# Performance work log

Measured on AMD Instinct MI355X. Metric: run time of the kernel, lower is better.

The kernel has to match this reference:

```python
import jax, jax.numpy as jnp
import numpy as np

DIM = 2048
N_HEADS = 16
HEAD_DIM = 128
EPS = 1e-6


def setup_inputs() -> dict:
    key = jax.random.key(0)
    ks = jax.random.split(key, 8)
    b, gf, gh, gw = 1, 8, 16, 24
    s = gf * gh * gw
    c = HEAD_DIM // 2
    w = lambda k: 0.02 * jax.random.normal(k, (DIM, DIM), jnp.float32)
    return {
        "x": jax.random.normal(ks[0], (b, s, DIM), jnp.float32),
        "freqs_angle": jax.random.normal(ks[1], (1024, c), jnp.float32),
        "Wq": w(ks[2]), "bq": jnp.zeros((DIM,), jnp.float32),
        "Wk": w(ks[3]), "bk": jnp.zeros((DIM,), jnp.float32),
        "Wv": w(ks[4]), "bv": jnp.zeros((DIM,), jnp.float32),
        "Wo": w(ks[5]), "bo": jnp.zeros((DIM,), jnp.float32),
        "gq": jnp.ones((DIM,), jnp.float32),
        "gk": jnp.ones((DIM,), jnp.float32),
        "seq_len": s, "grid_f": gf, "grid_h": gh, "grid_w": gw,
    }


def _rms(t, g):
    return t * jax.lax.rsqrt(jnp.mean(t * t, axis=-1, keepdims=True) + EPS) * g


def _grid_angles(freqs_angle, gf, gh, gw, c):
    # band split [c - 2*(c//3), c//3, c//3] as in rope_apply
    cf = c - 2 * (c // 3)
    ch = cw = c // 3
    af = freqs_angle[:gf, :cf]            # [F, cf]
    ah = freqs_angle[:gh, cf:cf + ch]     # [H, ch]
    aw = freqs_angle[:gw, cf + ch:c]      # [W, cw]
    ang = jnp.concatenate([
        jnp.broadcast_to(af[:, None, None, :], (gf, gh, gw, cf)),
        jnp.broadcast_to(ah[None, :, None, :], (gf, gh, gw, ch)),
        jnp.broadcast_to(aw[None, None, :, :], (gf, gh, gw, cw)),
    ], axis=-1)
    return ang.reshape(gf * gh * gw, c)   # [s, c]


def reference(x, freqs_angle, Wq, bq, Wk, bk, Wv, bv, Wo, bo, gq, gk,
              seq_len, grid_f, grid_h, grid_w):
    b, s, _ = x.shape
    n, d = N_HEADS, HEAD_DIM
    c = d // 2
    ang = _grid_angles(freqs_angle, grid_f, grid_h, grid_w, c)
    cos = jnp.cos(ang)[None, :, None, :]  # [1, s, 1, c]
    sin = jnp.sin(ang)[None, :, None, :]

    def rope(t):  # complex multiply on (even, odd) = (real, imag) pairs
        te, to = t[..., 0::2], t[..., 1::2]
        return jnp.stack([te * cos - to * sin, te * sin + to * cos], axis=-1).reshape(t.shape)

    q = _rms(x @ Wq.T + bq, gq).reshape(b, s, n, d)
    k = _rms(x @ Wk.T + bk, gk).reshape(b, s, n, d)
    v = (x @ Wv.T + bv).reshape(b, s, n, d)
    q, k = rope(q), rope(k)

    scale = np.float32(1.0 / np.sqrt(d))
    scores = jnp.einsum('bqnd,bknd->bnqk', q, k) * scale
    p = jax.nn.softmax(scores, axis=-1)
    o = jnp.einsum('bnqk,bknd->bqnd', p, v).reshape(b, s, n * d)
    return o @ Wo.T + bo
```

## Files before the change

### kernel.cpp

```cpp
#include <hip/hip_runtime.h>
#include <stdint.h>
#include <stddef.h>

typedef __bf16 bf16_t;
typedef __bf16 bf16x8 __attribute__((ext_vector_type(8)));
typedef __bf16 bf16x4 __attribute__((ext_vector_type(4)));
typedef __bf16 bf16x2 __attribute__((ext_vector_type(2)));
typedef float  f32x4  __attribute__((ext_vector_type(4)));

#define SEQ   3072
#define DIMD  2048
#define NH    16
#define HD    128
#define QKVN  6144

__device__ __forceinline__ void async16(const bf16_t* g, bf16_t* l) {
  __builtin_amdgcn_global_load_lds((const __attribute__((address_space(1))) uint32_t*)g,
                                   (__attribute__((address_space(3))) uint32_t*)l, 16, 0, 0);
}

__global__ __launch_bounds__(256) void cvt_all(const float* __restrict__ x,
                                               const float* __restrict__ Wq,
                                               const float* __restrict__ Wk,
                                               const float* __restrict__ Wv,
                                               const float* __restrict__ Wo,
                                               const float* __restrict__ bq,
                                               const float* __restrict__ bk,
                                               const float* __restrict__ bv,
                                               bf16_t* __restrict__ xb,
                                               bf16_t* __restrict__ Wqkvb,
                                               bf16_t* __restrict__ Wob,
                                               float* __restrict__ bqkv) {
  const int b = blockIdx.x;
  const float* src; bf16_t* dst; int off;
  if (b < 3072)       { src = x;  dst = xb;              off = b; }
  else if (b < 5120)  { src = Wq; dst = Wqkvb;           off = b - 3072; }
  else if (b < 7168)  { src = Wk; dst = Wqkvb + 4194304; off = b - 5120; }
  else if (b < 9216)  { src = Wv; dst = Wqkvb + 8388608; off = b - 7168; }
  else if (b < 11264) { src = Wo; dst = Wob;             off = b - 9216; }
  else {
    int t = (b - 11264) * 256 + threadIdx.x;
    float v;
    if (t < 2048)      v = bq[t];
    else if (t < 4096) v = bk[t - 2048];
    else               v = bv[t - 4096];
    bqkv[t] = v;
    return;
  }
  const int idx = (off * 256 + threadIdx.x) * 8;
  const float4 a = *(const float4*)(src + idx);
  const float4 c = *(const float4*)(src + idx + 4);
  bf16x8 o;
  o[0] = (bf16_t)a.x; o[1] = (bf16_t)a.y; o[2] = (bf16_t)a.z; o[3] = (bf16_t)a.w;
  o[4] = (bf16_t)c.x; o[5] = (bf16_t)c.y; o[6] = (bf16_t)c.z; o[7] = (bf16_t)c.w;
  *(bf16x8*)(dst + idx) = o;
}

template<bool OUT_BF16>
__global__ __launch_bounds__(256, 2) void gemm_nt(const bf16_t* __restrict__ A,
                                                  const bf16_t* __restrict__ B,
                                                  const float* __restrict__ bias,
                                                  void* __restrict__ Cout,
                                                  int M, int N, int K) {
  __shared__ __align__(16) bf16_t As[128 * 64];
  __shared__ __align__(16) bf16_t Bs[128 * 64];
  const int t = threadIdx.x;
  const int lane = t & 63, wave = t >> 6;
  const int quad = lane >> 4, l15 = lane & 15;
  const int wy = wave >> 1, wx = wave & 1;
  const size_t bm = (size_t)blockIdx.y * 128, bn = (size_t)blockIdx.x * 128;
  const bf16_t* Ab = A + bm * K;
  const bf16_t* Bb = B + bn * K;
  f32x4 acc[4][4] = {};
  int srow[4], scol[4];
#pragma unroll
  for (int r = 0; r < 4; r++) {
    int L = r * 256 + t;
    int row = L >> 3, cp = L & 7;
    srow[r] = row;
    scol[r] = (cp ^ (row & 7)) * 8;
  }
  for (int k0 = 0; k0 < K; k0 += 64) {
    __syncthreads();
#pragma unroll
    for (int r = 0; r < 4; r++)
      async16(Ab + (size_t)srow[r] * K + k0 + scol[r], &As[(r * 256 + t) * 8]);
#pragma unroll
    for (int r = 0; r < 4; r++)
      async16(Bb + (size_t)srow[r] * K + k0 + scol[r], &Bs[(r * 256 + t) * 8]);
    __syncthreads();
#pragma unroll
    for (int ks = 0; ks < 2; ks++) {
      bf16x8 af[4], bfv[4];
#pragma unroll
      for (int i = 0; i < 4; i++) {
        int row = wy * 64 + i * 16 + l15;
        af[i] = *(const bf16x8*)&As[row * 64 + (((ks * 4 + quad) ^ (row & 7)) * 8)];
      }
#pragma unroll
      for (int j = 0; j < 4; j++) {
        int row = wx * 64 + j * 16 + l15;
        bfv[j] = *(const bf16x8*)&Bs[row * 64 + (((ks * 4 + quad) ^ (row & 7)) * 8)];
      }
#pragma unroll
      for (int i = 0; i < 4; i++)
#pragma unroll
        for (int j = 0; j < 4; j++)
          acc[i][j] = __builtin_amdgcn_mfma_f32_16x16x32_bf16(af[i], bfv[j], acc[i][j], 0, 0, 0);
    }
  }
#pragma unroll
  for (int i = 0; i < 4; i++) {
#pragma unroll
    for (int j = 0; j < 4; j++) {
      size_t row = bm + wy * 64 + i * 16 + quad * 4;
      size_t col = bn + wx * 64 + j * 16 + l15;
      float bb = bias[col];
#pragma unroll
      for (int r = 0; r < 4; r++) {
        float v = acc[i][j][r] + bb;
        if (OUT_BF16) ((bf16_t*)Cout)[(row + r) * N + col] = (bf16_t)v;
        else          ((float*)Cout)[(row + r) * N + col] = v;
      }
    }
  }
}

__global__ __launch_bounds__(256) void rmsrope(bf16_t* __restrict__ qkv,
                                               bf16_t* __restrict__ pk,
                                               const float* __restrict__ gq,
                                               const float* __restrict__ gk,
                                               const float* __restrict__ freqs) {
  const int s = blockIdx.x, t = threadIdx.x;
  bf16_t* row = qkv + (size_t)s * QKVN;
  bf16x8 qv = *(const bf16x8*)&row[t * 8];
  bf16x8 kv = *(const bf16x8*)&row[2048 + t * 8];
  float qf[8], kf[8];
  float qs = 0.f, ks2 = 0.f;
#pragma unroll
  for (int i = 0; i < 8; i++) {
    qf[i] = (float)qv[i]; qs  += qf[i] * qf[i];
    kf[i] = (float)kv[i]; ks2 += kf[i] * kf[i];
  }
#pragma unroll
  for (int m = 1; m < 64; m <<= 1) {
    qs  += __shfl_xor(qs, m);
    ks2 += __shfl_xor(ks2, m);
  }
  __shared__ float red[2][4];
  const int wave = t >> 6, lane = t & 63;
  if (lane == 0) { red[0][wave] = qs; red[1][wave] = ks2; }
  __syncthreads();
  qs  = red[0][0] + red[0][1] + red[0][2] + red[0][3];
  ks2 = red[1][0] + red[1][1] + red[1][2] + red[1][3];
  const float qsc = rsqrtf(qs  / 2048.f + 1e-6f) * 0.12751745f;
  const float ksc = rsqrtf(ks2 / 2048.f + 1e-6f);
  const int sf = s / 384, rem = s - sf * 384;
  const int sh = rem / 24, sw = rem - sh * 24;
  bf16x8 qo, ko;
#pragma unroll
  for (int u = 0; u < 4; u++) {
    const int col = t * 8 + 2 * u;
    const int i = (col >> 1) & 63;
    const int frow = (i < 22) ? sf : ((i < 43) ? sh : sw);
    const float ang = freqs[frow * 64 + i];
    float sn, cs;
    __sincosf(ang, &sn, &cs);
    float te = qf[2 * u]     * qsc * gq[col];
    float to = qf[2 * u + 1] * qsc * gq[col + 1];
    qo[2 * u]     = (bf16_t)(te * cs - to * sn);
    qo[2 * u + 1] = (bf16_t)(te * sn + to * cs);
    te = kf[2 * u]     * ksc * gk[col];
    to = kf[2 * u + 1] * ksc * gk[col + 1];
    ko[2 * u]     = (bf16_t)(te * cs - to * sn);
    ko[2 * u + 1] = (bf16_t)(te * sn + to * cs);
  }
  *(bf16x8*)&row[t * 8] = qo;
  *(bf16x8*)&pk[((size_t)(t >> 4) * SEQ + s) * HD + (t & 15) * 8] = ko;
}

__global__ __launch_bounds__(256) void vtrans(const bf16_t* __restrict__ qkv,
                                              bf16_t* __restrict__ pvt) {
  __shared__ bf16_t tile[128][65];
  const int h = blockIdx.y;
  const int s0 = blockIdx.x * 64;
  const int t = threadIdx.x;
#pragma unroll
  for (int r = 0; r < 4; r++) {
    int L = r * 256 + t, s = L >> 4, cp = L & 15;
    bf16x8 v = *(const bf16x8*)&qkv[(size_t)(s0 + s) * QKVN + 4096 + h * HD + cp * 8];
#pragma unroll
    for (int i = 0; i < 8; i++) tile[cp * 8 + i][s] = v[i];
  }
  __syncthreads();
#pragma unroll
  for (int r = 0; r < 4; r++) {
    int L = r * 256 + t, d = L >> 3, c = L & 7;
    bf16x8 o;
#pragma unroll
    for (int i = 0; i < 8; i++) o[i] = tile[d][c * 8 + i];
    *(bf16x8*)&pvt[((size_t)h * HD + d) * SEQ + s0 + c * 8] = o;
  }
}

#define STAGE_KV(BUF, KV1) do {                                              \
    _Pragma("unroll")                                                        \
    for (int r = 0; r < 5; r++) {                                            \
      int L = r * 192 + t;                                                   \
      async16(pkh + (size_t)(KV1) * HD + koff[r], &Ks[BUF][L * 8]);          \
      async16(pvh + (KV1) + voff[r], &Vt[BUF][L * 8]);                       \
    }                                                                        \
    if (t < 64) {                                                            \
      int L = 5 * 192 + t;                                                   \
      async16(pkh + (size_t)(KV1) * HD + koff[5], &Ks[BUF][L * 8]);          \
      async16(pvh + (KV1) + voff[5], &Vt[BUF][L * 8]);                       \
    }                                                                        \
  } while (0)

__global__ __launch_bounds__(192, 2) void flash_attn(const bf16_t* __restrict__ qkv,
                                                     const bf16_t* __restrict__ pk,
                                                     const bf16_t* __restrict__ pvt,
                                                     bf16_t* __restrict__ ob) {
  __shared__ __align__(16) bf16_t Ks[2][64 * 128];
  __shared__ __align__(16) bf16_t Vt[2][128 * 64];
  __shared__ __align__(16) bf16_t Ps[3][32 * 64];
  const int h = blockIdx.y, qt = blockIdx.x;
  const int s0 = qt * 96;
  const int t = threadIdx.x, wave = t >> 6, lane = t & 63;
  const int quad = lane >> 4, l15 = lane & 15;
  const int wq = wave * 32;
  const bf16_t* pkh = pk  + (size_t)h * (SEQ * HD);
  const bf16_t* pvh = pvt + (size_t)h * (HD * SEQ);
  int koff[6], voff[6];
#pragma unroll
  for (int r = 0; r < 6; r++) {
    int L = r * 192 + t;
    int krow = L >> 4, kc = (L & 15) ^ (krow & 7);
    koff[r] = krow * HD + kc * 8;
    int vd = L >> 3, vc = (L & 7) ^ (vd & 7);
    voff[r] = vd * SEQ + vc * 8;
  }
  bf16x8 qfr[2][4];
#pragma unroll
  for (int tj = 0; tj < 2; tj++)
#pragma unroll
    for (int ks = 0; ks < 4; ks++)
      qfr[tj][ks] = *(const bf16x8*)&qkv[(size_t)(s0 + wq + tj * 16 + l15) * QKVN + h * HD + ks * 32 + quad * 8];
  f32x4 oacc[2][8] = {};
  float m_run[2] = {-3e38f, -3e38f}, l_run[2] = {0.f, 0.f};
  STAGE_KV(0, 0);
  for (int kt = 0; kt < SEQ / 64; kt++) {
    const int cur = kt & 1;
    __syncthreads();
    if (kt + 1 < SEQ / 64) STAGE_KV(cur ^ 1, (kt + 1) * 64);
    f32x4 st[4][2] = {};
#pragma unroll
    for (int ks = 0; ks < 4; ks++) {
      bf16x8 kfr[4];
#pragma unroll
      for (int ti = 0; ti < 4; ti++) {
        const int kr = ti * 16 + l15;
        kfr[ti] = *(const bf16x8*)&Ks[cur][kr * 128 + (((ks * 4 + quad) ^ (kr & 7)) * 8)];
      }
#pragma unroll
      for (int ti = 0; ti < 4; ti++)
#pragma unroll
        for (int tj = 0; tj < 2; tj++)
          st[ti][tj] = __builtin_amdgcn_mfma_f32_16x16x32_bf16(kfr[ti], qfr[tj][ks], st[ti][tj], 0, 0, 0);
    }
    float mt[2] = {-3e38f, -3e38f};
#pragma unroll
    for (int ti = 0; ti < 4; ti++)
#pragma unroll
      for (int tj = 0; tj < 2; tj++)
#pragma unroll
        for (int r = 0; r < 4; r++)
          mt[tj] = fmaxf(mt[tj], st[ti][tj][r]);
    float al[2]; bool resc[2];
#pragma unroll
    for (int tj = 0; tj < 2; tj++) {
      mt[tj] = fmaxf(mt[tj], __shfl_xor(mt[tj], 16));
      mt[tj] = fmaxf(mt[tj], __shfl_xor(mt[tj], 32));
      if (__all(mt[tj] <= m_run[tj] + 11.5f)) {
        al[tj] = 1.f; resc[tj] = false;
      } else {
        const float mn = fmaxf(m_run[tj], mt[tj]);
        al[tj] = __builtin_amdgcn_exp2f(m_run[tj] - mn);
        m_run[tj] = mn;
        resc[tj] = true;
      }
    }
    float lt[2] = {0.f, 0.f};
#pragma unroll
    for (int ti = 0; ti < 4; ti++)
#pragma unroll
      for (int tj = 0; tj < 2; tj++) {
        bf16x4 pv;
#pragma unroll
        for (int r = 0; r < 4; r++) {
          const float p = __builtin_amdgcn_exp2f(st[ti][tj][r] - m_run[tj]);
          pv[r] = (bf16_t)p;
          lt[tj] += (float)pv[r];
        }
        const int q = tj * 16 + l15;
        const int cp2 = (ti * 2 + (quad >> 1)) ^ (q & 7);
        *(bf16x4*)&Ps[wave][q * 64 + cp2 * 8 + (quad & 1) * 4] = pv;
      }
#pragma unroll
    for (int tj = 0; tj < 2; tj++) {
      lt[tj] += __shfl_xor(lt[tj], 16);
      lt[tj] += __shfl_xor(lt[tj], 32);
      l_run[tj] = l_run[tj] * al[tj] + lt[tj];
    }
#pragma unroll
    for (int ti = 0; ti < 2; ti++) {
      if (resc[ti]) {
        float a0 = __shfl(al[ti], quad * 4 + 0);
        float a1 = __shfl(al[ti], quad * 4 + 1);
        float a2 = __shfl(al[ti], quad * 4 + 2);
        float a3 = __shfl(al[ti], quad * 4 + 3);
#pragma unroll
        for (int dj = 0; dj < 8; dj++) {
          oacc[ti][dj][0] *= a0; oacc[ti][dj][1] *= a1;
          oacc[ti][dj][2] *= a2; oacc[ti][dj][3] *= a3;
        }
      }
    }
#pragma unroll
    for (int ks = 0; ks < 2; ks++) {
      bf16x8 pf[2], vf[8];
#pragma unroll
      for (int ti = 0; ti < 2; ti++) {
        const int q = ti * 16 + l15;
        pf[ti] = *(const bf16x8*)&Ps[wave][q * 64 + (((ks * 4 + quad) ^ (q & 7)) * 8)];
      }
#pragma unroll
      for (int dj = 0; dj < 8; dj++) {
        const int d = dj * 16 + l15;
        vf[dj] = *(const bf16x8*)&Vt[cur][d * 64 + (((ks * 4 + quad) ^ (d & 7)) * 8)];
      }
#pragma unroll
      for (int ti = 0; ti < 2; ti++)
#pragma unroll
        for (int dj = 0; dj < 8; dj++)
          oacc[ti][dj] = __builtin_amdgcn_mfma_f32_16x16x32_bf16(pf[ti], vf[dj], oacc[ti][dj], 0, 0, 0);
    }
  }
#pragma unroll
  for (int ti = 0; ti < 2; ti++) {
    float li[4];
#pragma unroll
    for (int r = 0; r < 4; r++) li[r] = 1.f / __shfl(l_run[ti], quad * 4 + r);
#pragma unroll
    for (int dj = 0; dj < 8; dj++)
#pragma unroll
      for (int r = 0; r < 4; r++) {
        const float v = oacc[ti][dj][r] * li[r];
        ob[(size_t)(s0 + wq + ti * 16 + quad * 4 + r) * DIMD + h * HD + dj * 16 + l15] = (bf16_t)v;
      }
  }
}

extern "C" void kernel_launch(void* const* d_in, const int* in_sizes, int n_in,
                              void* d_out, int out_size, void* d_ws, size_t ws_size,
                              hipStream_t stream) {
  (void)in_sizes; (void)n_in; (void)out_size;
  const float* x     = (const float*)d_in[0];
  const float* freqs = (const float*)d_in[1];
  const float* Wq    = (const float*)d_in[2];
  const float* bq    = (const float*)d_in[3];
  const float* Wk    = (const float*)d_in[4];
  const float* bk    = (const float*)d_in[5];
  const float* Wv    = (const float*)d_in[6];
  const float* bv    = (const float*)d_in[7];
  const float* Wo    = (const float*)d_in[8];
  const float* bo    = (const float*)d_in[9];
  const float* gq    = (const float*)d_in[10];
  const float* gk    = (const float*)d_in[11];

  char* w = (char*)d_ws;
  bf16_t* xb    = (bf16_t*)(w);
  bf16_t* Wqkvb = (bf16_t*)(w + 12582912);
  bf16_t* Wob   = (bf16_t*)(w + 37748736);
  bf16_t* qkvb  = (bf16_t*)(w + 46137344);
  bf16_t* obuf  = (bf16_t*)(w + 83886080);
  float*  bqkv  = (float*) (w + 96468992);
  bf16_t* pk    = (bf16_t*)(w);
  bf16_t* pvt   = (bf16_t*)(w + 12582912);
  if (ws_size < (size_t)96493568) return;

  cvt_all<<<11288, 256, 0, stream>>>(x, Wq, Wk, Wv, Wo, bq, bk, bv, xb, Wqkvb, Wob, bqkv);

  gemm_nt<true><<<dim3(48, 24), 256, 0, stream>>>(xb, Wqkvb, bqkv, qkvb, SEQ, QKVN, DIMD);
  rmsrope<<<3072, 256, 0, stream>>>(qkvb, pk, gq, gk, freqs);
  vtrans<<<dim3(48, NH), 256, 0, stream>>>(qkvb, pvt);
  flash_attn<<<dim3(32, NH), 192, 0, stream>>>(qkvb, pk, pvt, obuf);
  gemm_nt<false><<<dim3(16, 24), 256, 0, stream>>>(obuf, Wob, bo, (float*)d_out, SEQ, DIMD, DIMD);
}
```

Measured before the change: 432.8 us.

## Switch flash attention to 32x32x16 MFMA with register-resident P and MFMA row sums

Rewrites the attention inner loop to use 32x32x16 bf16 MFMAs, computing S^T so the probability tile can be rearranged into A-operand fragments in registers with cross-half lane shuffles. This drops the per-wave P shared-memory round trip and its bank traffic. The row-sum is computed by an extra MFMA against a ones vector rather than scalar adds and shuffles, and s_setprio hints are added around the MFMA phases. The cost is more accumulator registers (f32x16 tiles) and an extra MFMA per PV step, which may hurt occupancy at two blocks per CU.

```diff
diff --git a/kernel.cpp b/kernel.cpp
--- a/kernel.cpp
+++ b/kernel.cpp
@@ -7,6 +7,7 @@
 typedef __bf16 bf16x4 __attribute__((ext_vector_type(4)));
 typedef __bf16 bf16x2 __attribute__((ext_vector_type(2)));
 typedef float  f32x4  __attribute__((ext_vector_type(4)));
+typedef float  f32x16 __attribute__((ext_vector_type(16)));
 
 #define SEQ   3072
 #define DIMD  2048
@@ -223,14 +224,13 @@
                                                      bf16_t* __restrict__ ob) {
   __shared__ __align__(16) bf16_t Ks[2][64 * 128];
   __shared__ __align__(16) bf16_t Vt[2][128 * 64];
-  __shared__ __align__(16) bf16_t Ps[3][32 * 64];
-  const int h = blockIdx.y, qt = blockIdx.x;
+  const int hh = blockIdx.y, qt = blockIdx.x;
   const int s0 = qt * 96;
   const int t = threadIdx.x, wave = t >> 6, lane = t & 63;
-  const int quad = lane >> 4, l15 = lane & 15;
+  const int l31 = lane & 31, hl = lane >> 5;
   const int wq = wave * 32;
-  const bf16_t* pkh = pk  + (size_t)h * (SEQ * HD);
-  const bf16_t* pvh = pvt + (size_t)h * (HD * SEQ);
+  const bf16_t* pkh = pk  + (size_t)hh * (SEQ * HD);
+  const bf16_t* pvh = pvt + (size_t)hh * (HD * SEQ);
   int koff[6], voff[6];
 #pragma unroll
   for (int r = 0; r < 6; r++) {
@@ -240,124 +240,101 @@
     int vd = L >> 3, vc = (L & 7) ^ (vd & 7);
     voff[r] = vd * SEQ + vc * 8;
   }
-  bf16x8 qfr[2][4];
-#pragma unroll
-  for (int tj = 0; tj < 2; tj++)
-#pragma unroll
-    for (int ks = 0; ks < 4; ks++)
-      qfr[tj][ks] = *(const bf16x8*)&qkv[(size_t)(s0 + wq + tj * 16 + l15) * QKVN + h * HD + ks * 32 + quad * 8];
-  f32x4 oacc[2][8] = {};
-  float m_run[2] = {-3e38f, -3e38f}, l_run[2] = {0.f, 0.f};
+  bf16x8 qfr[8];
+#pragma unroll
+  for (int ks = 0; ks < 8; ks++)
+    qfr[ks] = *(const bf16x8*)&qkv[(size_t)(s0 + wq + l31) * QKVN + hh * HD + ks * 16 + hl * 8];
+  bf16x8 vones;
+#pragma unroll
+  for (int i = 0; i < 8; i++) vones[i] = (bf16_t)1.0f;
+  f32x16 oacc[4] = {};
+  f32x16 lacc = {};
+  float m_run = -3e38f;
   STAGE_KV(0, 0);
   for (int kt = 0; kt < SEQ / 64; kt++) {
     const int cur = kt & 1;
     __syncthreads();
     if (kt + 1 < SEQ / 64) STAGE_KV(cur ^ 1, (kt + 1) * 64);
-    f32x4 st[4][2] = {};
-#pragma unroll
-    for (int ks = 0; ks < 4; ks++) {
-      bf16x8 kfr[4];
-#pragma unroll
-      for (int ti = 0; ti < 4; ti++) {
-        const int kr = ti * 16 + l15;
-        kfr[ti] = *(const bf16x8*)&Ks[cur][kr * 128 + (((ks * 4 + quad) ^ (kr & 7)) * 8)];
+    f32x16 st0 = {}, st1 = {};
+    __builtin_amdgcn_s_setprio(1);
+#pragma unroll
+    for (int ks = 0; ks < 8; ks++) {
+      const int r1 = 32 + l31;
+      bf16x8 k0 = *(const bf16x8*)&Ks[cur][l31 * 128 + (((ks * 2 + hl) ^ (l31 & 7)) * 8)];
+      bf16x8 k1 = *(const bf16x8*)&Ks[cur][r1 * 128 + (((ks * 2 + hl) ^ (r1 & 7)) * 8)];
+      st0 = __builtin_amdgcn_mfma_f32_32x32x16_bf16(k0, qfr[ks], st0, 0, 0, 0);
+      st1 = __builtin_amdgcn_mfma_f32_32x32x16_bf16(k1, qfr[ks], st1, 0, 0, 0);
+    }
+    __builtin_amdgcn_s_setprio(0);
+    float mt = st0[0];
+#pragma unroll
+    for (int r = 1; r < 16; r++) mt = fmaxf(mt, st0[r]);
+#pragma unroll
+    for (int r = 0; r < 16; r++) mt = fmaxf(mt, st1[r]);
+    mt = fmaxf(mt, __shfl_xor(mt, 32));
+    if (!__all(mt <= m_run + 11.5f)) {
+      const float mn = fmaxf(m_run, mt);
+      const float al = __builtin_amdgcn_exp2f(m_run - mn);
+      m_run = mn;
+#pragma unroll
+      for (int r = 0; r < 16; r++) {
+        const float a = __shfl(al, (r & 3) + 8 * (r >> 2) + 4 * hl);
+        lacc[r] *= a;
+#pragma unroll
+        for (int dj = 0; dj < 4; dj++) oacc[dj][r] *= a;
       }
-#pragma unroll
-      for (int ti = 0; ti < 4; ti++)
-#pragma unroll
-        for (int tj = 0; tj < 2; tj++)
-          st[ti][tj] = __builtin_amdgcn_mfma_f32_16x16x32_bf16(kfr[ti], qfr[tj][ks], st[ti][tj], 0, 0, 0);
-    }
-    float mt[2] = {-3e38f, -3e38f};
-#pragma unroll
-    for (int ti = 0; ti < 4; ti++)
-#pragma unroll
-      for (int tj = 0; tj < 2; tj++)
-#pragma unroll
-        for (int r = 0; r < 4; r++)
-          mt[tj] = fmaxf(mt[tj], st[ti][tj][r]);
-    float al[2]; bool resc[2];
-#pragma unroll
-    for (int tj = 0; tj < 2; tj++) {
-      mt[tj] = fmaxf(mt[tj], __shfl_xor(mt[tj], 16));
-      mt[tj] = fmaxf(mt[tj], __shfl_xor(mt[tj], 32));
-      if (__all(mt[tj] <= m_run[tj] + 11.5f)) {
-        al[tj] = 1.f; resc[tj] = false;
-      } else {
-        const float mn = fmaxf(m_run[tj], mt[tj]);
-        al[tj] = __builtin_amdgcn_exp2f(m_run[tj] - mn);
-        m_run[tj] = mn;
-        resc[tj] = true;
-      }
-    }
-    float lt[2] = {0.f, 0.f};
-#pragma unroll
-    for (int ti = 0; ti < 4; ti++)
-#pragma unroll
-      for (int tj = 0; tj < 2; tj++) {
-        bf16x4 pv;
-#pragma unroll
-        for (int r = 0; r < 4; r++) {
-          const float p = __builtin_amdgcn_exp2f(st[ti][tj][r] - m_run[tj]);
-          pv[r] = (bf16_t)p;
-          lt[tj] += (float)pv[r];
-        }
-        const int q = tj * 16 + l15;
-        const int cp2 = (ti * 2 + (quad >> 1)) ^ (q & 7);
-        *(bf16x4*)&Ps[wave][q * 64 + cp2 * 8 + (quad & 1) * 4] = pv;
-      }
-#pragma unroll
-    for (int tj = 0; tj < 2; tj++) {
-      lt[tj] += __shfl_xor(lt[tj], 16);
-      lt[tj] += __shfl_xor(lt[tj], 32);
-      l_run[tj] = l_run[tj] * al[tj] + lt[tj];
-    }
-#pragma unroll
-    for (int ti = 0; ti < 2; ti++) {
-      if (resc[ti]) {
-        float a0 = __shfl(al[ti], quad * 4 + 0);
-        float a1 = __shfl(al[ti], quad * 4 + 1);
-        float a2 = __shfl(al[ti], quad * 4 + 2);
-        float a3 = __shfl(al[ti], quad * 4 + 3);
-#pragma unroll
-        for (int dj = 0; dj < 8; dj++) {
-          oacc[ti][dj][0] *= a0; oacc[ti][dj][1] *= a1;
-          oacc[ti][dj][2] *= a2; oacc[ti][dj][3] *= a3;
-        }
-      }
-    }
-#pragma unroll
-    for (int ks = 0; ks < 2; ks++) {
-      bf16x8 pf[2], vf[8];
-#pragma unroll
-      for (int ti = 0; ti < 2; ti++) {
-        const int q = ti * 16 + l15;
-        pf[ti] = *(const bf16x8*)&Ps[wave][q * 64 + (((ks * 4 + quad) ^ (q & 7)) * 8)];
-      }
-#pragma unroll
-      for (int dj = 0; dj < 8; dj++) {
-        const int d = dj * 16 + l15;
-        vf[dj] = *(const bf16x8*)&Vt[cur][d * 64 + (((ks * 4 + quad) ^ (d & 7)) * 8)];
-      }
-#pragma unroll
-      for (int ti = 0; ti < 2; ti++)
-#pragma unroll
-        for (int dj = 0; dj < 8; dj++)
-          oacc[ti][dj] = __builtin_amdgcn_mfma_f32_16x16x32_bf16(pf[ti], vf[dj], oacc[ti][dj], 0, 0, 0);
-    }
-  }
-#pragma unroll
-  for (int ti = 0; ti < 2; ti++) {
-    float li[4];
-#pragma unroll
-    for (int r = 0; r < 4; r++) li[r] = 1.f / __shfl(l_run[ti], quad * 4 + r);
-#pragma unroll
-    for (int dj = 0; dj < 8; dj++)
-#pragma unroll
-      for (int r = 0; r < 4; r++) {
-        const float v = oacc[ti][dj][r] * li[r];
-        ob[(size_t)(s0 + wq + ti * 16 + quad * 4 + r) * DIMD + h * HD + dj * 16 + l15] = (bf16_t)v;
-      }
+    }
+    uint32_t c0[8], c1[8];
+#pragma unroll
+    for (int m = 0; m < 8; m++) {
+      bf16x2 w0, w1;
+      w0[0] = (bf16_t)__builtin_amdgcn_exp2f(st0[2 * m]     - m_run);
+      w0[1] = (bf16_t)__builtin_amdgcn_exp2f(st0[2 * m + 1] - m_run);
+      w1[0] = (bf16_t)__builtin_amdgcn_exp2f(st1[2 * m]     - m_run);
+      w1[1] = (bf16_t)__builtin_amdgcn_exp2f(st1[2 * m + 1] - m_run);
+      c0[m] = __builtin_bit_cast(uint32_t, w0);
+      c1[m] = __builtin_bit_cast(uint32_t, w1);
+    }
+    union U8 { uint32_t u[4]; bf16x8 v; } afr0, afr1, afr2, afr3;
+#define BUILD_AFR(DST, CB, B) do {                                           \
+      uint32_t sA = hl ? CB[(B) + 0] : CB[(B) + 2];                          \
+      uint32_t sB = hl ? CB[(B) + 1] : CB[(B) + 3];                          \
+      uint32_t rA = (uint32_t)__shfl_xor((int)sA, 32);                       \
+      uint32_t rB = (uint32_t)__shfl_xor((int)sB, 32);                       \
+      DST.u[0] = hl ? rA : CB[(B) + 0];                                      \
+      DST.u[1] = hl ? rB : CB[(B) + 1];                                      \
+      DST.u[2] = hl ? CB[(B) + 2] : rA;                                      \
+      DST.u[3] = hl ? CB[(B) + 3] : rB;                                      \
+    } while (0)
+    BUILD_AFR(afr0, c0, 0);
+    BUILD_AFR(afr1, c0, 4);
+    BUILD_AFR(afr2, c1, 0);
+    BUILD_AFR(afr3, c1, 4);
+#undef BUILD_AFR
+    __builtin_amdgcn_s_setprio(1);
+#define PV_STEP(AFR, S) do {                                                            \
+      lacc = __builtin_amdgcn_mfma_f32_32x32x16_bf16(AFR.v, vones, lacc, 0, 0, 0);      \
+      _Pragma("unroll")                                                                 \
+      for (int dj = 0; dj < 4; dj++) {                                                  \
+        const int row = dj * 32 + l31;                                                  \
+        bf16x8 vf = *(const bf16x8*)&Vt[cur][row * 64 + ((((S) * 2 + hl) ^ (row & 7)) * 8)]; \
+        oacc[dj] = __builtin_amdgcn_mfma_f32_32x32x16_bf16(AFR.v, vf, oacc[dj], 0, 0, 0);    \
+      }                                                                                 \
+    } while (0)
+    PV_STEP(afr0, 0);
+    PV_STEP(afr1, 1);
+    PV_STEP(afr2, 2);
+    PV_STEP(afr3, 3);
+#undef PV_STEP
+    __builtin_amdgcn_s_setprio(0);
+  }
+#pragma unroll
+  for (int r = 0; r < 16; r++) {
+    const float li = 1.f / lacc[r];
+    const size_t row = (size_t)(s0 + wq + (r & 3) + 8 * (r >> 2) + 4 * hl);
+#pragma unroll
+    for (int dj = 0; dj < 4; dj++)
+      ob[row * DIMD + hh * HD + dj * 32 + l31] = (bf16_t)(oacc[dj][r] * li);
   }
 }
 
```

Measured after the change: 422.2 us. -2.4%, faster.
